# Kernel tuning notes

Measured on AMD Instinct MI355X. Metric: run time of the kernel, lower is better.

## Reference

```python
import jax, jax.numpy as jnp
import numpy as np

FP8_MAX = 448.0  # max finite value of float8_e4m3fn


def setup_inputs() -> dict:
    key = jax.random.key(0)
    k1, k2, k3 = jax.random.split(key, 3)
    B, S, D_IN, D_OUT = 2, 4096, 2048, 8192
    x = jax.random.normal(k1, (B, S, D_IN), dtype=jnp.float32)
    # Weight is stored pre-quantized in fp8 (per-tensor scale), layout (in, out)
    w_fp32 = jax.random.normal(k2, (D_IN, D_OUT), dtype=jnp.float32) * 0.02
    weight_scale = jnp.float32(jnp.max(jnp.abs(w_fp32)) / FP8_MAX)
    weight = jnp.clip(w_fp32 / weight_scale, -FP8_MAX, FP8_MAX).astype(jnp.float8_e4m3fn)
    input_scale = jnp.float32(0.05)  # static per-tensor activation scale
    bias = jax.random.normal(k3, (D_OUT,), dtype=jnp.float32)
    return {"x": x, "weight": weight, "weight_scale": weight_scale,
            "input_scale": input_scale, "bias": bias}


def reference(x, weight, weight_scale, input_scale, bias):
    # static_quantize_e4m3_per_tensor: q = cast_fp8(clip(x / s)), returns (q, s)
    q = jnp.clip(x / input_scale, -FP8_MAX, FP8_MAX).astype(jnp.float8_e4m3fn)
    q2d = q.reshape(-1, q.shape[-1]).astype(jnp.float32)  # [B*S, D_in]
    w = weight.astype(jnp.float32)                         # [D_in, D_out]
    # cublas_scaled_mm: (q @ w) * scale_a * scale_b, out in x.dtype
    out = jnp.matmul(q2d, w) * (input_scale * weight_scale)
    out = out.astype(x.dtype) + bias.astype(x.dtype)
    return out.reshape(x.shape[:-1] + (out.shape[-1],))
```

## Files before the change

### kernel.cpp

```cpp
#include <hip/hip_runtime.h>

typedef __attribute__((ext_vector_type(4)))  float floatx4;
typedef __attribute__((ext_vector_type(16))) float floatx16;
typedef __attribute__((ext_vector_type(8)))  int   intx8;

__device__ __forceinline__ unsigned int pack4_fp8(float f0, float f1, float f2, float f3) {
    int v = __builtin_amdgcn_cvt_pk_fp8_f32(f0, f1, 0, false);
    v = __builtin_amdgcn_cvt_pk_fp8_f32(f2, f3, v, true);
    return (unsigned int)v;
}

__device__ __forceinline__ void gload16(const unsigned char* g, unsigned char* l) {
    __builtin_amdgcn_global_load_lds(
        (const __attribute__((address_space(1))) unsigned int*)g,
        (__attribute__((address_space(3))) unsigned int*)l, 16, 0, 0);
}

__global__ void detect_kernel(const unsigned int* __restrict__ W, int* __restrict__ flag) {
    __shared__ int ok[2];
    if (threadIdx.x == 0) { ok[0] = 1; ok[1] = 1; }
    __syncthreads();
    int f32ok = 1, bf16ok = 1;
#pragma unroll
    for (int i = 0; i < 16; ++i) {
        unsigned int w = W[threadIdx.x * 16 + i];
        if (w & 0x000FFFFFu) f32ok = 0;
        if (w & 0x000F000Fu) bf16ok = 0;
    }
    if (!f32ok)  atomicAnd(&ok[0], 0);
    if (!bf16ok) atomicAnd(&ok[1], 0);
    __syncthreads();
    if (threadIdx.x == 0) *flag = ok[0] ? 2 : (ok[1] ? 1 : 0);
}

__global__ void quant_kernel(const float* __restrict__ x,
                             unsigned int* __restrict__ q,
                             const float* __restrict__ iscale, int n8) {
    int i = blockIdx.x * blockDim.x + threadIdx.x;
    if (i >= n8) return;
    float s = iscale[0];
    const float4* xv = (const float4*)x;
    float4 a = xv[2 * i];
    float4 b = xv[2 * i + 1];
    float v[8] = {a.x, a.y, a.z, a.w, b.x, b.y, b.z, b.w};
#pragma unroll
    for (int j = 0; j < 8; ++j) {
        float t = v[j] / s;
        v[j] = fminf(fmaxf(t, -448.0f), 448.0f);
    }
    q[2 * i]     = pack4_fp8(v[0], v[1], v[2], v[3]);
    q[2 * i + 1] = pack4_fp8(v[4], v[5], v[6], v[7]);
}

template <int MODE>
__device__ __forceinline__ void ingest_body(const unsigned char* __restrict__ W,
                                            unsigned char* __restrict__ Wt,
                                            int K, int N,
                                            unsigned char (*tile)[68]) {
    const int k0 = blockIdx.y * 64;
    const int n0 = blockIdx.x * 64;
    const int t = threadIdx.x;
    const int kr = t >> 2;
    const int cg = (t & 3) * 16;
    const size_t eidx = (size_t)(k0 + kr) * N + (n0 + cg);

    unsigned int w4[4];
    if constexpr (MODE == 0) {
        uint4 v = *(const uint4*)(W + eidx);
        w4[0] = v.x; w4[1] = v.y; w4[2] = v.z; w4[3] = v.w;
    } else if constexpr (MODE == 1) {
        const uint4* p = (const uint4*)((const unsigned short*)W + eidx);
        uint4 A0 = p[0], A1 = p[1];
        unsigned int uw[8] = {A0.x, A0.y, A0.z, A0.w, A1.x, A1.y, A1.z, A1.w};
#pragma unroll
        for (int g = 0; g < 4; ++g) {
            float f0 = __uint_as_float((uw[2 * g] & 0xFFFFu) << 16);
            float f1 = __uint_as_float((uw[2 * g] >> 16) << 16);
            float f2 = __uint_as_float((uw[2 * g + 1] & 0xFFFFu) << 16);
            float f3 = __uint_as_float((uw[2 * g + 1] >> 16) << 16);
            w4[g] = pack4_fp8(f0, f1, f2, f3);
        }
    } else {
        const float4* p = (const float4*)((const float*)W + eidx);
#pragma unroll
        for (int g = 0; g < 4; ++g) {
            float4 f = p[g];
            w4[g] = pack4_fp8(f.x, f.y, f.z, f.w);
        }
    }
#pragma unroll
    for (int g = 0; g < 4; ++g)
        *(unsigned int*)&tile[kr][cg + 4 * g] = w4[g];
    __syncthreads();

    const int nr = t >> 2;
    const int kg = (t & 3) * 16;
    uint4 o;
    unsigned int w[4];
#pragma unroll
    for (int g = 0; g < 4; ++g) {
        unsigned int b0 = tile[kg + g * 4 + 0][nr];
        unsigned int b1 = tile[kg + g * 4 + 1][nr];
        unsigned int b2 = tile[kg + g * 4 + 2][nr];
        unsigned int b3 = tile[kg + g * 4 + 3][nr];
        w[g] = b0 | (b1 << 8) | (b2 << 16) | (b3 << 24);
    }
    o.x = w[0]; o.y = w[1]; o.z = w[2]; o.w = w[3];
    *(uint4*)(Wt + (size_t)(n0 + nr) * K + k0 + kg) = o;
}

__global__ void ingest_kernel(const unsigned char* __restrict__ W,
                              unsigned char* __restrict__ Wt,
                              const int* __restrict__ flag, int K, int N) {
    __shared__ __align__(16) unsigned char tile[64][68];
    const int mode = *flag;
    if (mode == 0)      ingest_body<0>(W, Wt, K, N, tile);
    else if (mode == 1) ingest_body<1>(W, Wt, K, N, tile);
    else                ingest_body<2>(W, Wt, K, N, tile);
}

__global__ __launch_bounds__(512, 2) void gemm_mxfp8_kernel(
    const unsigned char* __restrict__ A,
    const unsigned char* __restrict__ Bt,
    float* __restrict__ C,
    const float* __restrict__ bias,
    const float* __restrict__ wscale,
    const float* __restrict__ iscale,
    int M, int N, int K) {
    __shared__ __align__(16) unsigned char As[2 * 32768];
    __shared__ __align__(16) unsigned char Bs[2 * 32768];

    const int tid  = threadIdx.x;
    const int lane = tid & 63;
    const int wv   = tid >> 6;
    const int wm   = wv >> 2;
    const int wn   = wv & 3;
    const int r16  = lane & 15;
    const int cq   = lane >> 4;

    const int bm = blockIdx.y * 256;
    const int bn = blockIdx.x * 256;

    const unsigned char* ga[4];
    const unsigned char* gb[4];
    int lo[4];
#pragma unroll
    for (int j = 0; j < 4; ++j) {
        const int u   = wv * 4 + j;
        const int rb  = u >> 1;
        const int rg  = u & 1;
        const int row = rb * 16 + r16;
        const int col = cq * 32 + rg * 16;
        ga[j] = A  + (size_t)(bm + row) * K + col;
        gb[j] = Bt + (size_t)(bn + row) * K + col;
        lo[j] = u * 1024;
    }

    floatx16 acc[4][2] = {};
    const int NT = K >> 7;

    const int labase = ((lane >> 4) & 1) * 2048 + (lane & 15) * 16 + (lane >> 5) * 256;

#pragma unroll
    for (int j = 0; j < 4; ++j) {
        gload16(ga[j], &As[lo[j]]);
        gload16(gb[j], &Bs[lo[j]]);
        ga[j] += 128; gb[j] += 128;
    }
    if (NT > 1) {
#pragma unroll
        for (int j = 0; j < 4; ++j) {
            gload16(gb[j], &Bs[32768 + lo[j]]);
            gb[j] += 128;
        }
        asm volatile("s_waitcnt vmcnt(4)" ::: "memory");
    } else {
        asm volatile("s_waitcnt vmcnt(0)" ::: "memory");
    }
    __builtin_amdgcn_s_barrier();
    __builtin_amdgcn_sched_barrier(0);

    union U8 { intx8 v; uint4 q[2]; };

#define READ_FRAG(dst, p)                                           \
    do {                                                            \
        U8 _u;                                                      \
        _u.q[0] = *(const uint4*)(p);                               \
        _u.q[1] = *(const uint4*)((p) + 1024);                      \
        (dst) = _u.v;                                               \
    } while (0)

#define MFMA4(afA, afB, mA, mB, b0_, b1_)                                   \
    do {                                                                    \
        __builtin_amdgcn_s_setprio(1);                                      \
        acc[mA][0] = __builtin_amdgcn_mfma_scale_f32_32x32x64_f8f6f4(       \
            afA, b0_, acc[mA][0], 0, 0, 0, 0x7F7F7F7F, 0, 0x7F7F7F7F);      \
        acc[mA][1] = __builtin_amdgcn_mfma_scale_f32_32x32x64_f8f6f4(       \
            afA, b1_, acc[mA][1], 0, 0, 0, 0x7F7F7F7F, 0, 0x7F7F7F7F);      \
        acc[mB][0] = __builtin_amdgcn_mfma_scale_f32_32x32x64_f8f6f4(       \
            afB, b0_, acc[mB][0], 0, 0, 0, 0x7F7F7F7F, 0, 0x7F7F7F7F);      \
        acc[mB][1] = __builtin_amdgcn_mfma_scale_f32_32x32x64_f8f6f4(       \
            afB, b1_, acc[mB][1], 0, 0, 0, 0x7F7F7F7F, 0, 0x7F7F7F7F);      \
        __builtin_amdgcn_s_setprio(0);                                      \
    } while (0)

#define PHASE_WAIT()                                             \
    do {                                                         \
        __builtin_amdgcn_s_barrier();                            \
        asm volatile("s_waitcnt lgkmcnt(0)" ::: "memory");       \
        __builtin_amdgcn_sched_barrier(0);                       \
    } while (0)

    for (int kt = 0; kt < NT; ++kt) {
        const unsigned char* Ab = &As[(kt & 1) * 32768];
        const unsigned char* Bb = &Bs[(kt & 1) * 32768];
        unsigned char* An  = &As[((kt + 1) & 1) * 32768];
        unsigned char* Bn2 = &Bs[(kt & 1) * 32768];
        const bool pfA = (kt + 1 < NT);
        const bool pfB = (kt + 2 < NT);

        const unsigned char* aB = Ab + labase;
        const unsigned char* bB = Bb + labase;
        intx8 b00, b01, b10, b11, af0, af1;

        READ_FRAG(b00, bB + (wn * 4 + 0) * 2048);
        READ_FRAG(b01, bB + (wn * 4 + 2) * 2048);
        READ_FRAG(af0, aB + (wm * 8 + 0) * 2048);
        READ_FRAG(af1, aB + (wm * 8 + 2) * 2048);
        if (pfA) {
            gload16(ga[0], An + lo[0]); gload16(ga[1], An + lo[1]);
            ga[0] += 128; ga[1] += 128;
        }
        PHASE_WAIT();
        MFMA4(af0, af1, 0, 1, b00, b01);
        __builtin_amdgcn_s_barrier();

        READ_FRAG(b10, bB + (wn * 4 + 0) * 2048 + 512);
        READ_FRAG(b11, bB + (wn * 4 + 2) * 2048 + 512);
        READ_FRAG(af0, aB + (wm * 8 + 4) * 2048);
        READ_FRAG(af1, aB + (wm * 8 + 6) * 2048);
        if (pfA) {
            gload16(ga[2], An + lo[2]); gload16(ga[3], An + lo[3]);
            ga[2] += 128; ga[3] += 128;
        }
        PHASE_WAIT();
        MFMA4(af0, af1, 2, 3, b00, b01);
        __builtin_amdgcn_s_barrier();

        READ_FRAG(af0, aB + (wm * 8 + 0) * 2048 + 512);
        READ_FRAG(af1, aB + (wm * 8 + 2) * 2048 + 512);
        if (pfB) {
            gload16(gb[0], Bn2 + lo[0]); gload16(gb[1], Bn2 + lo[1]);
            gb[0] += 128; gb[1] += 128;
        }
        PHASE_WAIT();
        MFMA4(af0, af1, 0, 1, b10, b11);
        __builtin_amdgcn_s_barrier();

        READ_FRAG(af0, aB + (wm * 8 + 4) * 2048 + 512);
        READ_FRAG(af1, aB + (wm * 8 + 6) * 2048 + 512);
        if (pfB) {
            gload16(gb[2], Bn2 + lo[2]); gload16(gb[3], Bn2 + lo[3]);
            gb[2] += 128; gb[3] += 128;
        }
        PHASE_WAIT();
        MFMA4(af0, af1, 2, 3, b10, b11);
        if (pfB) {
            asm volatile("s_waitcnt vmcnt(4)" ::: "memory");
        } else {
            asm volatile("s_waitcnt vmcnt(0)" ::: "memory");
        }
        __builtin_amdgcn_s_barrier();
        __builtin_amdgcn_sched_barrier(0);
    }
    (void)M; (void)r16; (void)cq;
#undef READ_FRAG
#undef MFMA4
#undef PHASE_WAIT

    const float scale = iscale[0] * wscale[0];
    const int colb = bn + wn * 64 + (lane & 31);
    const float bv0 = bias[colb];
    const float bv1 = bias[colb + 32];
    const int rowb = bm + wm * 128 + 4 * (lane >> 5);
#pragma unroll
    for (int mb = 0; mb < 4; ++mb) {
#pragma unroll
        for (int r = 0; r < 16; ++r) {
            const int row = rowb + mb * 32 + (r & 3) + 8 * (r >> 2);
            float* cp = C + (size_t)row * N + colb;
            cp[0]  = acc[mb][0][r] * scale + bv0;
            cp[32] = acc[mb][1][r] * scale + bv1;
        }
    }
}

extern "C" void kernel_launch(void* const* d_in, const int* in_sizes, int n_in,
                              void* d_out, int out_size, void* d_ws, size_t ws_size,
                              hipStream_t stream) {
    const float* x          = (const float*)d_in[0];
    const unsigned char* w  = (const unsigned char*)d_in[1];
    const float* wscale     = (const float*)d_in[2];
    const float* iscale     = (const float*)d_in[3];
    const float* bias       = (const float*)d_in[4];
    float* out              = (float*)d_out;

    const int D_OUT = in_sizes[4];
    const int D_IN  = in_sizes[1] / D_OUT;
    const int M     = in_sizes[0] / D_IN;

    int* flag         = (int*)d_ws;
    unsigned char* q  = (unsigned char*)d_ws + 256;
    unsigned char* wt = q + (size_t)M * D_IN;

    detect_kernel<<<1, 256, 0, stream>>>((const unsigned int*)w, flag);
    const int n8 = (M * D_IN) / 8;
    quant_kernel<<<(n8 + 255) / 256, 256, 0, stream>>>(x, (unsigned int*)q, iscale, n8);
    dim3 tg(D_OUT / 64, D_IN / 64);
    ingest_kernel<<<tg, 256, 0, stream>>>(w, wt, flag, D_IN, D_OUT);
    gemm_mxfp8_kernel<<<dim3(D_OUT / 256, M / 256), 512, 0, stream>>>(
        q, wt, out, bias, wscale, iscale, M, D_OUT, D_IN);
}
```

Measured before the change: 507.4 us.

## Replace phased barrier pipeline with simple double-buffered prefetch loop

Drops the four-phase schedule, which split the prefetches for each K tile and placed a workgroup barrier and an lgkmcnt wait before every MFMA group. The new loop issues all A and B global-to-LDS loads for the next tile up front into the alternate buffer, then reads fragments with extra registers and interleaves them with the MFMAs. There is now only one vmcnt wait and one barrier per iteration. This reduces barrier and synchronization overhead and lets the compiler overlap LDS reads with MFMAs, at the cost of more live registers and less finely staged global loads.

```diff
diff --git a/kernel.cpp b/kernel.cpp
--- a/kernel.cpp
+++ b/kernel.cpp
@@ -167,16 +167,7 @@
         gload16(gb[j], &Bs[lo[j]]);
         ga[j] += 128; gb[j] += 128;
     }
-    if (NT > 1) {
-#pragma unroll
-        for (int j = 0; j < 4; ++j) {
-            gload16(gb[j], &Bs[32768 + lo[j]]);
-            gb[j] += 128;
-        }
-        asm volatile("s_waitcnt vmcnt(4)" ::: "memory");
-    } else {
-        asm volatile("s_waitcnt vmcnt(0)" ::: "memory");
-    }
+    asm volatile("s_waitcnt vmcnt(0)" ::: "memory");
     __builtin_amdgcn_s_barrier();
     __builtin_amdgcn_sched_barrier(0);
 
@@ -204,79 +195,55 @@
         __builtin_amdgcn_s_setprio(0);                                      \
     } while (0)
 
-#define PHASE_WAIT()                                             \
-    do {                                                         \
-        __builtin_amdgcn_s_barrier();                            \
-        asm volatile("s_waitcnt lgkmcnt(0)" ::: "memory");       \
-        __builtin_amdgcn_sched_barrier(0);                       \
-    } while (0)
-
     for (int kt = 0; kt < NT; ++kt) {
         const unsigned char* Ab = &As[(kt & 1) * 32768];
         const unsigned char* Bb = &Bs[(kt & 1) * 32768];
-        unsigned char* An  = &As[((kt + 1) & 1) * 32768];
-        unsigned char* Bn2 = &Bs[(kt & 1) * 32768];
-        const bool pfA = (kt + 1 < NT);
-        const bool pfB = (kt + 2 < NT);
+        unsigned char* An = &As[((kt + 1) & 1) * 32768];
+        unsigned char* Bn = &Bs[((kt + 1) & 1) * 32768];
+
+        if (kt + 1 < NT) {
+#pragma unroll
+            for (int j = 0; j < 4; ++j) {
+                gload16(ga[j], An + lo[j]);
+                gload16(gb[j], Bn + lo[j]);
+                ga[j] += 128; gb[j] += 128;
+            }
+        }
+        __builtin_amdgcn_sched_barrier(0);
 
         const unsigned char* aB = Ab + labase;
         const unsigned char* bB = Bb + labase;
-        intx8 b00, b01, b10, b11, af0, af1;
+        intx8 b00, b01, b10, b11, af0, af1, ag0, ag1;
 
         READ_FRAG(b00, bB + (wn * 4 + 0) * 2048);
         READ_FRAG(b01, bB + (wn * 4 + 2) * 2048);
         READ_FRAG(af0, aB + (wm * 8 + 0) * 2048);
         READ_FRAG(af1, aB + (wm * 8 + 2) * 2048);
-        if (pfA) {
-            gload16(ga[0], An + lo[0]); gload16(ga[1], An + lo[1]);
-            ga[0] += 128; ga[1] += 128;
-        }
-        PHASE_WAIT();
-        MFMA4(af0, af1, 0, 1, b00, b01);
-        __builtin_amdgcn_s_barrier();
-
         READ_FRAG(b10, bB + (wn * 4 + 0) * 2048 + 512);
         READ_FRAG(b11, bB + (wn * 4 + 2) * 2048 + 512);
-        READ_FRAG(af0, aB + (wm * 8 + 4) * 2048);
-        READ_FRAG(af1, aB + (wm * 8 + 6) * 2048);
-        if (pfA) {
-            gload16(ga[2], An + lo[2]); gload16(ga[3], An + lo[3]);
-            ga[2] += 128; ga[3] += 128;
-        }
-        PHASE_WAIT();
-        MFMA4(af0, af1, 2, 3, b00, b01);
-        __builtin_amdgcn_s_barrier();
+        READ_FRAG(ag0, aB + (wm * 8 + 4) * 2048);
+        READ_FRAG(ag1, aB + (wm * 8 + 6) * 2048);
+
+        MFMA4(af0, af1, 0, 1, b00, b01);
 
         READ_FRAG(af0, aB + (wm * 8 + 0) * 2048 + 512);
         READ_FRAG(af1, aB + (wm * 8 + 2) * 2048 + 512);
-        if (pfB) {
-            gload16(gb[0], Bn2 + lo[0]); gload16(gb[1], Bn2 + lo[1]);
-            gb[0] += 128; gb[1] += 128;
-        }
-        PHASE_WAIT();
+
+        MFMA4(ag0, ag1, 2, 3, b00, b01);
+
+        READ_FRAG(ag0, aB + (wm * 8 + 4) * 2048 + 512);
+        READ_FRAG(ag1, aB + (wm * 8 + 6) * 2048 + 512);
+
         MFMA4(af0, af1, 0, 1, b10, b11);
-        __builtin_amdgcn_s_barrier();
-
-        READ_FRAG(af0, aB + (wm * 8 + 4) * 2048 + 512);
-        READ_FRAG(af1, aB + (wm * 8 + 6) * 2048 + 512);
-        if (pfB) {
-            gload16(gb[2], Bn2 + lo[2]); gload16(gb[3], Bn2 + lo[3]);
-            gb[2] += 128; gb[3] += 128;
-        }
-        PHASE_WAIT();
-        MFMA4(af0, af1, 2, 3, b10, b11);
-        if (pfB) {
-            asm volatile("s_waitcnt vmcnt(4)" ::: "memory");
-        } else {
-            asm volatile("s_waitcnt vmcnt(0)" ::: "memory");
-        }
+        MFMA4(ag0, ag1, 2, 3, b10, b11);
+
+        asm volatile("s_waitcnt vmcnt(0)" ::: "memory");
         __builtin_amdgcn_s_barrier();
         __builtin_amdgcn_sched_barrier(0);
     }
     (void)M; (void)r16; (void)cq;
 #undef READ_FRAG
 #undef MFMA4
-#undef PHASE_WAIT
 
     const float scale = iscale[0] * wscale[0];
     const int colb = bn + wn * 64 + (lane & 31);
```

Result: slower. 537.5 us (+5.9%).
